# Kernel optimization log

Hardware: AMD Instinct MI355X
Metric: run time of the kernel (lower is better)

The kernel has to match this reference:

```python
import jax, jax.numpy as jnp
import numpy as np

D_MODEL = 1024
N_HEADS = 16
D_K = D_MODEL // N_HEADS
THETA = 10000.0
NEG_INF = -1e30


def _rope_tables(token_positions, d_k, theta=THETA):
    # freqs[t, i] = t / theta**(2i/d_k), i in [0, d_k/2)
    exponent = jnp.arange(0, d_k, 2, dtype=jnp.float32)  # [d_k/2]
    inv_freq = 1.0 / theta ** (exponent / d_k)
    freqs = token_positions.astype(jnp.float32)[:, None] * inv_freq[None, :]  # [s, d_k/2]
    return jnp.cos(freqs), jnp.sin(freqs)


def _apply_rope(x, cos, sin):
    # x: [..., s, d_k]; interleaved pair rotation (pairs are (x[2i], x[2i+1]))
    x1 = x[..., 0::2]
    x2 = x[..., 1::2]
    r1 = x1 * cos - x2 * sin
    r2 = x1 * sin + x2 * cos
    return jnp.stack([r1, r2], axis=-1).reshape(x.shape)


def setup_inputs() -> dict:
    key = jax.random.key(0)
    ks = jax.random.split(key, 5)
    b, s = 2, 2048
    scale = np.sqrt(2.0 / (D_MODEL + D_MODEL))
    return {
        "x": jax.random.normal(ks[0], (b, s, D_MODEL), dtype=jnp.float32),
        "Wq": jax.random.normal(ks[1], (D_MODEL, D_MODEL), dtype=jnp.float32) * scale,
        "Wk": jax.random.normal(ks[2], (D_MODEL, D_MODEL), dtype=jnp.float32) * scale,
        "Wv": jax.random.normal(ks[3], (D_MODEL, D_MODEL), dtype=jnp.float32) * scale,
        "Wo": jax.random.normal(ks[4], (D_MODEL, D_MODEL), dtype=jnp.float32) * scale,
        "token_positions": jnp.arange(s, dtype=jnp.int64 if jax.config.jax_enable_x64 else jnp.int32),
    }


def reference(x, Wq, Wk, Wv, Wo, token_positions):
    b, s, _ = x.shape
    # QKV projections: weight stored [in, out]
    q = jnp.einsum('bsi,io->bso', x, Wq)
    k = jnp.einsum('bsi,io->bso', x, Wk)
    v = jnp.einsum('bsi,io->bso', x, Wv)
    # split heads: [b, h, s, d_k]
    q = q.reshape(b, s, N_HEADS, D_K).transpose(0, 2, 1, 3)
    k = k.reshape(b, s, N_HEADS, D_K).transpose(0, 2, 1, 3)
    v = v.reshape(b, s, N_HEADS, D_K).transpose(0, 2, 1, 3)
    # RoPE
    cos, sin = _rope_tables(token_positions, D_K)
    q = _apply_rope(q, cos, sin)
    k = _apply_rope(k, cos, sin)
    # causal attention with full materialized scores (faithful to source)
    scores = jnp.einsum('bhid,bhjd->bhij', q, k) / jnp.sqrt(jnp.float32(D_K))
    mask = jnp.tril(jnp.ones((s, s), dtype=bool))
    scores = jnp.where(mask, scores, NEG_INF)
    probs = jax.nn.softmax(scores, axis=-1)
    out = jnp.einsum('bhij,bhjd->bhid', probs, v)
    out = out.transpose(0, 2, 1, 3).reshape(b, s, D_MODEL)
    return jnp.einsum('bsi,io->bso', out, Wo)
```

## Files before the change

kernel.cpp:

```cpp
#include <hip/hip_runtime.h>
#include <hip/hip_bf16.h>
#include <cmath>

#define S_LEN 2048
#define DMODEL 1024
#define NHEADS 16
#define DK 64
#define BATCH 2
#define MTOT (BATCH * S_LEN)

using short8 = __attribute__((ext_vector_type(8))) short;
using floatx4 = __attribute__((ext_vector_type(4))) float;

__device__ __forceinline__ unsigned short f2b(float f) {
    union { float f; unsigned u; } v; v.f = f;
    unsigned r = v.u + 0x7fff + ((v.u >> 16) & 1);
    return (unsigned short)(r >> 16);
}

__device__ __forceinline__ unsigned pack2(float a, float b) {
    float2 t; t.x = a; t.y = b;
    __hip_bfloat162 h = __float22bfloat162_rn(t);
    union { __hip_bfloat162 h; unsigned u; } v; v.h = h;
    return v.u;
}

__device__ __forceinline__ void gload16(const void* g, void* l) {
    __builtin_amdgcn_global_load_lds(
        (const __attribute__((address_space(1))) unsigned int*)g,
        (__attribute__((address_space(3))) unsigned int*)l, 16, 0, 0);
}

#define FENCE() asm volatile("" ::: "memory")

__global__ __launch_bounds__(256) void prep_k(
    const float* __restrict__ x, unsigned short* __restrict__ xb,
    const int* __restrict__ tokpos, float* __restrict__ ct, float* __restrict__ st,
    const float* W0, const float* W1, const float* W2, const float* W3,
    unsigned short* T0, unsigned short* T1, unsigned short* T2, unsigned short* T3) {
    __shared__ float t[64][65];
    const int b = blockIdx.x;
    if (b < 2048) {
        int i = (b * 256 + threadIdx.x) * 8;
        float4 a = *(const float4*)(x + i);
        float4 bb = *(const float4*)(x + i + 4);
        short8 o;
        o[0] = f2b(a.x); o[1] = f2b(a.y); o[2] = f2b(a.z); o[3] = f2b(a.w);
        o[4] = f2b(bb.x); o[5] = f2b(bb.y); o[6] = f2b(bb.z); o[7] = f2b(bb.w);
        *(short8*)(xb + i) = o;
    } else if (b < 2304) {
        int idx = (b - 2048) * 256 + threadIdx.x;
        int si = idx >> 5;
        int ip = idx & 31;
        float pos = (float)tokpos[si];
        float inv_freq = powf(10000.0f, -(float)(2 * ip) / 64.0f);
        float ang = pos * inv_freq;
        ct[idx] = cosf(ang);
        st[idx] = sinf(ang);
    } else {
        int id = b - 2304;
        int z = id >> 8;
        int bx = id & 15, by = (id >> 4) & 15;
        const float* W = z == 0 ? W0 : z == 1 ? W1 : z == 2 ? W2 : W3;
        unsigned short* T = z == 0 ? T0 : z == 1 ? T1 : z == 2 ? T2 : T3;
        const bool perm = (z < 2);
        int n0 = bx * 64, k0 = by * 64;
        int rr = threadIdx.x >> 6, cc = threadIdx.x & 63;
#pragma unroll
        for (int r = 0; r < 16; r++) {
            int row = r * 4 + rr;
            t[row][cc] = W[(size_t)(k0 + row) * DMODEL + n0 + cc];
        }
        __syncthreads();
#pragma unroll
        for (int r = 0; r < 16; r++) {
            int row = r * 4 + rr;
            int drow = perm ? (((row & 1) ? 32 : 0) + (row >> 1)) : row;
            T[(size_t)(n0 + drow) * DMODEL + k0 + cc] = f2b(t[cc][row]);
        }
    }
}

__global__ __launch_bounds__(256) void add_k(float* __restrict__ out,
                                             const float* __restrict__ p) {
    int i = (blockIdx.x * 256 + threadIdx.x) * 8;
    float4 a = *(const float4*)(out + i);
    float4 b = *(const float4*)(p + i);
    float4 c = *(const float4*)(out + i + 4);
    float4 d = *(const float4*)(p + i + 4);
    a.x += b.x; a.y += b.y; a.z += b.z; a.w += b.w;
    c.x += d.x; c.y += d.y; c.z += d.z; c.w += d.w;
    *(float4*)(out + i) = a;
    *(float4*)(out + i + 4) = c;
}

__global__ __launch_bounds__(512, 2) void mm_k(
    const unsigned short* __restrict__ A,
    const unsigned short* __restrict__ Bt0, const unsigned short* __restrict__ Bt1,
    const unsigned short* __restrict__ Bt2,
    void* C0, void* C1, void* C2,
    const float* __restrict__ ct, const float* __restrict__ st, int kind) {
    __shared__ __align__(16) unsigned short blob[10 * 8192];

    const int z = blockIdx.z;
    const unsigned short* Bt = (kind == 1) ? Bt0 : (z == 0 ? Bt0 : z == 1 ? Bt1 : Bt2);
    void* C = (kind == 1) ? (z == 0 ? C0 : C1) : (z == 0 ? C0 : z == 1 ? C1 : C2);
    const int mode = (kind == 1) ? 0 : (z == 2 ? 3 : 1);
    const int t0 = (kind == 1) ? z * 8 : 0;
    const int NT = (kind == 1) ? 8 : 16;
    const float qscale = (z == 0 && kind == 0) ? 0.18033688011112042f : 1.0f;

    const int tid = threadIdx.x;
    const int w = tid >> 6, lane = tid & 63;
    const int l15 = lane & 15, quad = lane >> 4;
    const int wr = w >> 2, wc = w & 3;
    const int m0 = blockIdx.x * 256, n0 = blockIdx.y * 256;

    const int rbase = (w >> 1) * 16 + l15;
    const int cbase = (w & 1) * 32 + quad * 8;

    floatx4 acc[8][4];
#pragma unroll
    for (int i = 0; i < 8; i++)
#pragma unroll
        for (int j = 0; j < 4; j++) acc[i][j] = (floatx4){0.f, 0.f, 0.f, 0.f};

    auto stage_half = [&](int h) {
        const int ts = t0 + (h >> 2), part = h & 3;
        const int slot = h % 10;
        const unsigned short* src =
            (part < 2 ? A + (((size_t)(m0 + part * 128 + rbase)) << 10)
                      : Bt + (((size_t)(n0 + (part - 2) * 128 + rbase)) << 10))
            + (size_t)ts * 64 + cbase;
        char* d = (char*)blob + slot * 16384 + w * 1024;
        gload16(src, d);
        gload16(src + (64 << 10), d + 8192);
    };

#pragma unroll
    for (int h = 0; h < 6; ++h) stage_half(h);
    asm volatile("s_waitcnt vmcnt(4)" ::: "memory");
    FENCE(); __builtin_amdgcn_s_barrier(); FENCE();

    short8 af[4][2];
    for (int t = 0; t < NT; ++t) {
        const int sb = (4 * t) % 10;
        int sA = sb + wr;            if (sA >= 10) sA -= 10;
        int sB = sb + 2 + (wc >> 1); if (sB >= 10) sB -= 10;
        const char* LA = (const char*)blob + sA * 16384;
        const char* LB = (const char*)blob + sB * 16384;
#pragma unroll
        for (int q = 0; q < 4; ++q) {
            const int rh = q >> 1, ch = q & 1;
            if (ch == 0) {
#pragma unroll
                for (int ii = 0; ii < 4; ++ii)
#pragma unroll
                    for (int kh = 0; kh < 2; ++kh)
                        af[ii][kh] = *(const short8*)(LA + ((rh * 4 + ii) * 2 + kh) * 1024 + lane * 16);
            }
            short8 bf[2][2];
#pragma unroll
            for (int jj = 0; jj < 2; ++jj)
#pragma unroll
                for (int kh = 0; kh < 2; ++kh)
                    bf[jj][kh] = *(const short8*)(LB + (((wc & 1) * 4 + ch * 2 + jj) * 2 + kh) * 1024 + lane * 16);
            const int h = 4 * t + q + 6;
            if (h < 4 * NT) stage_half(h);
            if (q == 3) {
                if (t == NT - 2) asm volatile("s_waitcnt vmcnt(0)" ::: "memory");
                else             asm volatile("s_waitcnt vmcnt(4)" ::: "memory");
            }
            FENCE(); __builtin_amdgcn_s_barrier(); FENCE();
            __builtin_amdgcn_s_setprio(1);
#pragma unroll
            for (int ii = 0; ii < 4; ++ii)
#pragma unroll
                for (int jj = 0; jj < 2; ++jj) {
                    floatx4 a0 = acc[rh * 4 + ii][ch * 2 + jj];
                    a0 = __builtin_amdgcn_mfma_f32_16x16x32_bf16(af[ii][0], bf[jj][0], a0, 0, 0, 0);
                    a0 = __builtin_amdgcn_mfma_f32_16x16x32_bf16(af[ii][1], bf[jj][1], a0, 0, 0, 0);
                    acc[rh * 4 + ii][ch * 2 + jj] = a0;
                }
            __builtin_amdgcn_s_setprio(0);
            FENCE(); __builtin_amdgcn_s_barrier(); FENCE();
        }
    }

#pragma unroll
    for (int i = 0; i < 8; i++) {
        const int rowb = m0 + wr * 128 + i * 16 + quad * 4;
        if (mode == 0) {
            float* Cf = (float*)C;
#pragma unroll
            for (int j = 0; j < 4; j++) {
                int colb = n0 + wc * 64 + j * 16 + l15;
#pragma unroll
                for (int r = 0; r < 4; r++)
                    Cf[(size_t)(rowb + r) * DMODEL + colb] = acc[i][j][r];
            }
        } else if (mode == 1) {
            unsigned short* Cb = (unsigned short*)C;
#pragma unroll
            for (int jh = 0; jh < 2; jh++) {
                int ip = jh * 16 + l15;
                int cole = n0 + wc * 64 + jh * 16 + l15;
#pragma unroll
                for (int r = 0; r < 4; r++) {
                    int row = rowb + r;
                    int si = row & (S_LEN - 1);
                    float c = ct[si * 32 + ip] * qscale;
                    float s = st[si * 32 + ip] * qscale;
                    float e = acc[i][jh][r];
                    float od = acc[i][jh + 2][r];
                    Cb[(size_t)row * DMODEL + cole] = f2b(e * c - od * s);
                    Cb[(size_t)row * DMODEL + cole + 32] = f2b(e * s + od * c);
                }
            }
        } else {
            unsigned short* Cb = (unsigned short*)C;
            const int bb2 = rowb >> 11;
            const int si = rowb & (S_LEN - 1);
#pragma unroll
            for (int j = 0; j < 4; j++) {
                int colb = n0 + wc * 64 + j * 16 + l15;
                ushort4 v;
                v.x = f2b(acc[i][j][0]); v.y = f2b(acc[i][j][1]);
                v.z = f2b(acc[i][j][2]); v.w = f2b(acc[i][j][3]);
                *(ushort4*)(Cb + (size_t)(bb2 * 1024 + colb) * S_LEN + si) = v;
            }
        }
    }
}

__global__ __launch_bounds__(512) void attn_k(const unsigned short* __restrict__ Q,
                                              const unsigned short* __restrict__ K,
                                              const unsigned short* __restrict__ Vt,
                                              unsigned short* __restrict__ O,
                                              float* __restrict__ Ub,
                                              float* __restrict__ MLb) {
    __shared__ __align__(16) unsigned short Kblob[2][4096];
    __shared__ __align__(16) unsigned short Vblob[2][4096];
    __shared__ __align__(16) unsigned short Ps[8][16 * 72];

    static const int T_qt[22] = {9, 8, 15, 15, 7, 14, 14, 13, 13, 6, 12,
                                 12, 11, 11, 5, 10, 10, 4, 3, 2, 1, 0};
    static const int T_k0[22] = {0, 0, 0, 16, 0, 0, 15, 0, 14, 0, 0,
                                 13, 0, 12, 0, 0, 11, 0, 0, 0, 0, 0};
    static const int T_k1[22] = {20, 18, 16, 32, 16, 15, 30, 14, 28, 14, 13,
                                 26, 12, 24, 12, 11, 22, 10, 8, 6, 4, 2};
    static const int T_sx[22] = {-1, -1, 10, 11, -1, 8, 9, 6, 7, -1, 4,
                                 5, 2, 3, -1, 0, 1, -1, -1, -1, -1, -1};

    const int tid = threadIdx.x;
    const int w = tid >> 6, lane = tid & 63;
    const int l15 = lane & 15, quad = lane >> 4;
    const int idx = blockIdx.x;
    const int sr = idx >> 5;
    const int bh = idx & 31;
    const int bb = bh >> 4, h = bh & 15;
    const int qt = T_qt[sr], kt0 = T_k0[sr], kt1 = T_k1[sr], sx = T_sx[sr];
    const int qbase = qt * 128 + w * 16;
    const int qrow = qbase + l15;

    const size_t qoff = (size_t)(bb * S_LEN + qbase + l15) * DMODEL + h * DK;
    short8 aq0 = *(const short8*)(Q + qoff + quad * 8);
    short8 aq1 = *(const short8*)(Q + qoff + 32 + quad * 8);

    floatx4 o[4];
#pragma unroll
    for (int f = 0; f < 4; f++) o[f] = (floatx4){0.f, 0.f, 0.f, 0.f};
    float mv = -1e30f, lv = 0.f;

    const unsigned short* Kb = K + (size_t)(bb * S_LEN) * DMODEL + h * DK;
    const unsigned short* Vb = Vt + (size_t)(bb * 1024 + h * DK) * S_LEN;
    unsigned short* ps = &Ps[w][0];

    auto stage = [&](int b, int kb) {
#pragma unroll
        for (int it = 0; it < 2; it++) {
            int g = it * 8 + w;
            if (g < 8) {
                const unsigned short* gp =
                    Kb + (size_t)(kb + (g >> 1) * 16 + l15) * DMODEL + (g & 1) * 32 + quad * 8;
                gload16(gp, (char*)&Kblob[b][0] + g * 1024);
            } else {
                int gv = g - 8;
                const unsigned short* gp =
                    Vb + (size_t)((gv >> 1) * 16 + l15) * S_LEN + kb + (gv & 1) * 32 + quad * 8;
                gload16(gp, (char*)&Vblob[b][0] + gv * 1024);
            }
        }
    };

    stage(0, kt0 * 64);
    for (int kt = kt0; kt < kt1; kt++) {
        const int b = (kt - kt0) & 1;
        const int kb = kt * 64;
        __syncthreads();
        if (kt + 1 < kt1) stage(b ^ 1, (kt + 1) * 64);

        if (kb <= qbase + 15) {
            const unsigned short* kbb = &Kblob[b][0];
            floatx4 c[4];
            __builtin_amdgcn_s_setprio(1);
#pragma unroll
            for (int g = 0; g < 4; g++) {
                short8 kf0 = *(const short8*)(kbb + (g * 2 + 0) * 512 + lane * 8);
                short8 kf1 = *(const short8*)(kbb + (g * 2 + 1) * 512 + lane * 8);
                floatx4 t = {0.f, 0.f, 0.f, 0.f};
                t = __builtin_amdgcn_mfma_f32_16x16x32_bf16(kf0, aq0, t, 0, 0, 0);
                c[g] = __builtin_amdgcn_mfma_f32_16x16x32_bf16(kf1, aq1, t, 0, 0, 0);
            }
            __builtin_amdgcn_s_setprio(0);

            float sv[16];
            if (kb + 63 <= qbase) {
#pragma unroll
                for (int g = 0; g < 4; g++)
#pragma unroll
                    for (int r = 0; r < 4; r++) sv[g * 4 + r] = c[g][r];
            } else {
#pragma unroll
                for (int g = 0; g < 4; g++)
#pragma unroll
                    for (int r = 0; r < 4; r++) {
                        int key = kb + g * 16 + quad * 4 + r;
                        sv[g * 4 + r] = (key <= qrow) ? c[g][r] : -1e30f;
                    }
            }
            float t0 = fmaxf(fmaxf(sv[0], sv[1]), sv[2]);
            float t1 = fmaxf(fmaxf(sv[3], sv[4]), sv[5]);
            float t2 = fmaxf(fmaxf(sv[6], sv[7]), sv[8]);
            float t3 = fmaxf(fmaxf(sv[9], sv[10]), sv[11]);
            float t4 = fmaxf(fmaxf(sv[12], sv[13]), sv[14]);
            float mx = fmaxf(fmaxf(fmaxf(t0, t1), fmaxf(t2, t3)), fmaxf(t4, sv[15]));
            mx = fmaxf(mx, __shfl_xor(mx, 16));
            mx = fmaxf(mx, __shfl_xor(mx, 32));

            if (!__all(mx <= mv)) {
                float mnew = fmaxf(mv, mx);
                float alpha = exp2f(mv - mnew);
                mv = mnew;
                lv *= alpha;
#pragma unroll
                for (int f = 0; f < 4; f++) {
                    o[f][0] *= alpha; o[f][1] *= alpha;
                    o[f][2] *= alpha; o[f][3] *= alpha;
                }
            }
            float p[16], psum = 0.f;
#pragma unroll
            for (int i = 0; i < 16; i++) {
                p[i] = exp2f(sv[i] - mv);
                psum += p[i];
            }
            lv += psum;

#pragma unroll
            for (int g = 0; g < 4; g++) {
                uint2 pk;
                pk.x = pack2(p[g * 4 + 0], p[g * 4 + 1]);
                pk.y = pack2(p[g * 4 + 2], p[g * 4 + 3]);
                *(uint2*)(ps + l15 * 72 + g * 16 + quad * 4) = pk;
            }
            short8 pf0 = *(const short8*)(ps + l15 * 72 + quad * 8);
            short8 pf1 = *(const short8*)(ps + l15 * 72 + 32 + quad * 8);
            const unsigned short* vbb = &Vblob[b][0];
            __builtin_amdgcn_s_setprio(1);
#pragma unroll
            for (int f = 0; f < 4; f++) {
                short8 vf0 = *(const short8*)(vbb + (f * 2 + 0) * 512 + lane * 8);
                short8 vf1 = *(const short8*)(vbb + (f * 2 + 1) * 512 + lane * 8);
                o[f] = __builtin_amdgcn_mfma_f32_16x16x32_bf16(vf0, pf0, o[f], 0, 0, 0);
                o[f] = __builtin_amdgcn_mfma_f32_16x16x32_bf16(vf1, pf1, o[f], 0, 0, 0);
            }
            __builtin_amdgcn_s_setprio(0);
        }
    }

    if (sx >= 0) {
        const int slot = sx * 32 + bh;
        float* up = Ub + (size_t)slot * 8192 + tid * 16;
#pragma unroll
        for (int f = 0; f < 4; f++) {
            float4 v; v.x = o[f][0]; v.y = o[f][1]; v.z = o[f][2]; v.w = o[f][3];
            *(float4*)(up + f * 4) = v;
        }
        float* mlp = MLb + (size_t)slot * 1024 + tid * 2;
        mlp[0] = mv;
        mlp[1] = lv;
    } else {
        lv += __shfl_xor(lv, 16);
        lv += __shfl_xor(lv, 32);
        float inv = 1.0f / lv;
        __syncthreads();
#pragma unroll
        for (int f = 0; f < 4; f++) {
            uint2 pk;
            pk.x = pack2(o[f][0] * inv, o[f][1] * inv);
            pk.y = pack2(o[f][2] * inv, o[f][3] * inv);
            *(uint2*)(ps + l15 * 72 + f * 16 + quad * 4) = pk;
        }
        short8 r0 = *(const short8*)(ps + l15 * 72 + quad * 8);
        short8 r1 = *(const short8*)(ps + l15 * 72 + 32 + quad * 8);
        size_t obase = (size_t)(bb * S_LEN + qbase + l15) * DMODEL + h * DK;
        *(short8*)(O + obase + quad * 8) = r0;
        *(short8*)(O + obase + 32 + quad * 8) = r1;
    }
}

__global__ __launch_bounds__(256) void mrg_k(const float* __restrict__ Ub,
                                             const float* __restrict__ MLb,
                                             unsigned short* __restrict__ O) {
    const int pid = blockIdx.x;
    const int qt = 10 + (pid >> 5);
    const int bh = pid & 31;
    const int bb = bh >> 4, h = bh & 15;
    const int slotA = ((qt - 10) * 2) * 32 + bh;
    const int slotB = slotA + 32;
    const int tid = threadIdx.x;
    const int q = tid >> 1, dh = tid & 1;
    const int tq = (q >> 4) * 64 + (q & 15);

    const float* mlA = MLb + (size_t)slotA * 1024;
    const float* mlB = MLb + (size_t)slotB * 1024;
    float mA = mlA[tq * 2], mB = mlB[tq * 2];
    float lA = 0.f, lB = 0.f;
#pragma unroll
    for (int qd = 0; qd < 4; qd++) {
        lA += mlA[(tq + qd * 16) * 2 + 1];
        lB += mlB[(tq + qd * 16) * 2 + 1];
    }
    float m = fmaxf(mA, mB);
    float wA = exp2f(mA - m), wB = exp2f(mB - m);
    float inv = 1.0f / (lA * wA + lB * wB);

    const float* uA = Ub + (size_t)slotA * 8192;
    const float* uB = Ub + (size_t)slotB * 8192;
    unsigned short ov[32];
#pragma unroll
    for (int dd = 0; dd < 32; dd++) {
        int d = dh * 32 + dd;
        int uoff = ((q >> 4) * 64 + ((d >> 2) & 3) * 16 + (q & 15)) * 16 + (d >> 4) * 4 + (d & 3);
        float v = (uA[uoff] * wA + uB[uoff] * wB) * inv;
        ov[dd] = f2b(v);
    }
    size_t obase = (size_t)(bb * S_LEN + qt * 128 + q) * DMODEL + h * DK + dh * 32;
#pragma unroll
    for (int c = 0; c < 4; c++)
        *(short8*)(O + obase + c * 8) = *(short8*)&ov[c * 8];
}

extern "C" void kernel_launch(void* const* d_in, const int* in_sizes, int n_in,
                              void* d_out, int out_size, void* d_ws,
                              size_t ws_size, hipStream_t stream) {
    const float* x = (const float*)d_in[0];
    const float* Wq = (const float*)d_in[1];
    const float* Wk = (const float*)d_in[2];
    const float* Wv = (const float*)d_in[3];
    const float* Wo = (const float*)d_in[4];
    const int* tokpos = (const int*)d_in[5];
    float* out = (float*)d_out;

    const size_t MD = (size_t)MTOT * DMODEL;
    const size_t WD = (size_t)DMODEL * DMODEL;
    unsigned short* xb = (unsigned short*)d_ws;
    unsigned short* Wqt = xb + MD;
    unsigned short* Wkt = Wqt + WD;
    unsigned short* Wvt = Wkt + WD;
    unsigned short* Wot = Wvt + WD;
    unsigned short* Q = Wot + WD;
    unsigned short* K = Q + MD;
    unsigned short* V = K + MD;
    unsigned short* Vt = V + MD;
    float* ct = (float*)(Vt + MD);
    float* st = ct + S_LEN * 32;
    unsigned short* O = V;
    float* P1 = (float*)Q;
    float* Ub = (float*)xb;
    float* MLb = Ub + (size_t)384 * 8192;

    prep_k<<<dim3(3328), dim3(256), 0, stream>>>(x, xb, tokpos, ct, st,
                                                 Wq, Wk, Wv, Wo, Wqt, Wkt, Wvt, Wot);

    mm_k<<<dim3(16, 4, 3), dim3(512), 0, stream>>>(xb, Wqt, Wkt, Wvt,
                                                   (void*)Q, (void*)K, (void*)Vt, ct, st, 0);
    attn_k<<<dim3(704), dim3(512), 0, stream>>>(Q, K, Vt, O, Ub, MLb);
    mrg_k<<<dim3(192), dim3(256), 0, stream>>>(Ub, MLb, O);
    mm_k<<<dim3(16, 4, 2), dim3(512), 0, stream>>>(O, Wot, Wot, Wot,
                                                   (void*)out, (void*)P1, (void*)P1, ct, st, 1);
    add_k<<<dim3(2048), dim3(256), 0, stream>>>(out, P1);
}
```

Baseline: 208.1 us.

## Shrink GEMM tiles to 128x256 with K-step 32 to double block count

Reworks the projection GEMM kernel to use 128-row tiles and 32-wide K steps instead of 256x256 tiles with 64-wide K. Shared memory per block is halved, launch bounds allow 4 blocks per CU, and the grid doubles so more of the GPU is busy on these small GEMMs. The staging ring and wait counts are restructured to match. In exchange, each block reuses its loaded data less, and the shorter K step means more barriers per unit of work.

```diff
diff --git a/kernel.cpp b/kernel.cpp
--- a/kernel.cpp
+++ b/kernel.cpp
@@ -94,102 +94,86 @@
     *(float4*)(out + i + 4) = c;
 }
 
-__global__ __launch_bounds__(512, 2) void mm_k(
+__global__ __launch_bounds__(512, 4) void mm_k(
     const unsigned short* __restrict__ A,
     const unsigned short* __restrict__ Bt0, const unsigned short* __restrict__ Bt1,
     const unsigned short* __restrict__ Bt2,
     void* C0, void* C1, void* C2,
     const float* __restrict__ ct, const float* __restrict__ st, int kind) {
-    __shared__ __align__(16) unsigned short blob[10 * 8192];
+    __shared__ __align__(16) unsigned short blob[10 * 4096];
 
     const int z = blockIdx.z;
     const unsigned short* Bt = (kind == 1) ? Bt0 : (z == 0 ? Bt0 : z == 1 ? Bt1 : Bt2);
     void* C = (kind == 1) ? (z == 0 ? C0 : C1) : (z == 0 ? C0 : z == 1 ? C1 : C2);
     const int mode = (kind == 1) ? 0 : (z == 2 ? 3 : 1);
-    const int t0 = (kind == 1) ? z * 8 : 0;
-    const int NT = (kind == 1) ? 8 : 16;
+    const int t0 = (kind == 1) ? z * 16 : 0;
+    const int NT = (kind == 1) ? 16 : 32;
     const float qscale = (z == 0 && kind == 0) ? 0.18033688011112042f : 1.0f;
 
     const int tid = threadIdx.x;
     const int w = tid >> 6, lane = tid & 63;
     const int l15 = lane & 15, quad = lane >> 4;
     const int wr = w >> 2, wc = w & 3;
-    const int m0 = blockIdx.x * 256, n0 = blockIdx.y * 256;
-
-    const int rbase = (w >> 1) * 16 + l15;
-    const int cbase = (w & 1) * 32 + quad * 8;
-
-    floatx4 acc[8][4];
-#pragma unroll
-    for (int i = 0; i < 8; i++)
+    const int m0 = blockIdx.x * 128, n0 = blockIdx.y * 256;
+
+    floatx4 acc[4][4];
+#pragma unroll
+    for (int i = 0; i < 4; i++)
 #pragma unroll
         for (int j = 0; j < 4; j++) acc[i][j] = (floatx4){0.f, 0.f, 0.f, 0.f};
 
-    auto stage_half = [&](int h) {
-        const int ts = t0 + (h >> 2), part = h & 3;
-        const int slot = h % 10;
+    auto stage = [&](int tt, int part) {
+        const int ts = t0 + tt;
+        const int slot = (3 * tt + part) % 10;
         const unsigned short* src =
-            (part < 2 ? A + (((size_t)(m0 + part * 128 + rbase)) << 10)
-                      : Bt + (((size_t)(n0 + (part - 2) * 128 + rbase)) << 10))
-            + (size_t)ts * 64 + cbase;
-        char* d = (char*)blob + slot * 16384 + w * 1024;
-        gload16(src, d);
-        gload16(src + (64 << 10), d + 8192);
+            (part == 0 ? A + ((size_t)(m0 + w * 16 + l15) << 10)
+                       : Bt + ((size_t)(n0 + (part - 1) * 128 + w * 16 + l15) << 10))
+            + ts * 32 + quad * 8;
+        gload16(src, (char*)blob + slot * 8192 + w * 1024);
     };
 
-#pragma unroll
-    for (int h = 0; h < 6; ++h) stage_half(h);
-    asm volatile("s_waitcnt vmcnt(4)" ::: "memory");
+    stage(0, 0); stage(0, 1); stage(0, 2);
+    stage(1, 0); stage(1, 1); stage(1, 2);
+    asm volatile("s_waitcnt vmcnt(3)" ::: "memory");
     FENCE(); __builtin_amdgcn_s_barrier(); FENCE();
 
-    short8 af[4][2];
     for (int t = 0; t < NT; ++t) {
-        const int sb = (4 * t) % 10;
-        int sA = sb + wr;            if (sA >= 10) sA -= 10;
-        int sB = sb + 2 + (wc >> 1); if (sB >= 10) sB -= 10;
-        const char* LA = (const char*)blob + sA * 16384;
-        const char* LB = (const char*)blob + sB * 16384;
-#pragma unroll
-        for (int q = 0; q < 4; ++q) {
-            const int rh = q >> 1, ch = q & 1;
-            if (ch == 0) {
-#pragma unroll
-                for (int ii = 0; ii < 4; ++ii)
-#pragma unroll
-                    for (int kh = 0; kh < 2; ++kh)
-                        af[ii][kh] = *(const short8*)(LA + ((rh * 4 + ii) * 2 + kh) * 1024 + lane * 16);
-            }
-            short8 bf[2][2];
-#pragma unroll
-            for (int jj = 0; jj < 2; ++jj)
-#pragma unroll
-                for (int kh = 0; kh < 2; ++kh)
-                    bf[jj][kh] = *(const short8*)(LB + (((wc & 1) * 4 + ch * 2 + jj) * 2 + kh) * 1024 + lane * 16);
-            const int h = 4 * t + q + 6;
-            if (h < 4 * NT) stage_half(h);
-            if (q == 3) {
+        int sA = (3 * t) % 10;
+        int sB = sA + 1 + (wc >> 1); if (sB >= 10) sB -= 10;
+        const char* LA = (const char*)blob + sA * 8192;
+        const char* LB = (const char*)blob + sB * 8192;
+#pragma unroll
+        for (int rh = 0; rh < 2; ++rh) {
+            short8 af[2], bf[4];
+#pragma unroll
+            for (int ii = 0; ii < 2; ++ii)
+                af[ii] = *(const short8*)(LA + (wr * 4 + rh * 2 + ii) * 1024 + lane * 16);
+#pragma unroll
+            for (int j = 0; j < 4; ++j)
+                bf[j] = *(const short8*)(LB + ((wc & 1) * 4 + j) * 1024 + lane * 16);
+            if (rh == 0) {
+                if (t + 2 < NT) { stage(t + 2, 0); stage(t + 2, 1); }
+            } else {
+                if (t + 2 < NT) stage(t + 2, 2);
                 if (t == NT - 2) asm volatile("s_waitcnt vmcnt(0)" ::: "memory");
-                else             asm volatile("s_waitcnt vmcnt(4)" ::: "memory");
+                else             asm volatile("s_waitcnt vmcnt(3)" ::: "memory");
             }
             FENCE(); __builtin_amdgcn_s_barrier(); FENCE();
             __builtin_amdgcn_s_setprio(1);
 #pragma unroll
-            for (int ii = 0; ii < 4; ++ii)
-#pragma unroll
-                for (int jj = 0; jj < 2; ++jj) {
-                    floatx4 a0 = acc[rh * 4 + ii][ch * 2 + jj];
-                    a0 = __builtin_amdgcn_mfma_f32_16x16x32_bf16(af[ii][0], bf[jj][0], a0, 0, 0, 0);
-                    a0 = __builtin_amdgcn_mfma_f32_16x16x32_bf16(af[ii][1], bf[jj][1], a0, 0, 0, 0);
-                    acc[rh * 4 + ii][ch * 2 + jj] = a0;
-                }
+            for (int ii = 0; ii < 2; ++ii)
+#pragma unroll
+                for (int j = 0; j < 4; ++j)
+                    acc[rh * 2 + ii][j] =
+                        __builtin_amdgcn_mfma_f32_16x16x32_bf16(af[ii], bf[j], acc[rh * 2 + ii][j], 0, 0, 0);
             __builtin_amdgcn_s_setprio(0);
             FENCE(); __builtin_amdgcn_s_barrier(); FENCE();
         }
     }
 
 #pragma unroll
-    for (int i = 0; i < 8; i++) {
-        const int rowb = m0 + wr * 128 + i * 16 + quad * 4;
+    for (int i = 0; i < 4; i++) {
+        const int rowb = m0 + wr * 64 + i * 16 + quad * 4;
         if (mode == 0) {
             float* Cf = (float*)C;
 #pragma unroll
@@ -219,7 +203,7 @@
             }
         } else {
             unsigned short* Cb = (unsigned short*)C;
-            const int bb2 = rowb >> 11;
+            const int bb2 = m0 >> 11;
             const int si = rowb & (S_LEN - 1);
 #pragma unroll
             for (int j = 0; j < 4; j++) {
@@ -484,11 +468,11 @@
     prep_k<<<dim3(3328), dim3(256), 0, stream>>>(x, xb, tokpos, ct, st,
                                                  Wq, Wk, Wv, Wo, Wqt, Wkt, Wvt, Wot);
 
-    mm_k<<<dim3(16, 4, 3), dim3(512), 0, stream>>>(xb, Wqt, Wkt, Wvt,
+    mm_k<<<dim3(32, 4, 3), dim3(512), 0, stream>>>(xb, Wqt, Wkt, Wvt,
                                                    (void*)Q, (void*)K, (void*)Vt, ct, st, 0);
     attn_k<<<dim3(704), dim3(512), 0, stream>>>(Q, K, Vt, O, Ub, MLb);
     mrg_k<<<dim3(192), dim3(256), 0, stream>>>(Ub, MLb, O);
-    mm_k<<<dim3(16, 4, 2), dim3(512), 0, stream>>>(O, Wot, Wot, Wot,
+    mm_k<<<dim3(32, 4, 2), dim3(512), 0, stream>>>(O, Wot, Wot, Wot,
                                                    (void*)out, (void*)P1, (void*)P1, ct, st, 1);
     add_k<<<dim3(2048), dim3(256), 0, stream>>>(out, P1);
 }
```

New measurement: 213.7 us. +2.7%, slower.
